# Performance work log

Measured on AMD Instinct MI355X. Metric: run time of the kernel, lower is better.

The kernel has to match this reference:

```python
import jax, jax.numpy as jnp
import numpy as np

HEADS = 8
EPS = 1e-5


def _layernorm(x, g, b):
    mu = jnp.mean(x, axis=-1, keepdims=True)
    var = jnp.mean(jnp.square(x - mu), axis=-1, keepdims=True)
    return (x - mu) * jax.lax.rsqrt(var + EPS) * g + b


def setup_inputs() -> dict:
    key = jax.random.key(0)
    ks = jax.random.split(key, 10)
    B, S, D = 4, 2048, 256
    d_ff = 2 * D
    s = 0.02
    return {
        "x": jax.random.normal(ks[0], (B, S, D), dtype=jnp.float32),
        "ln1_g": jnp.ones((D,), jnp.float32),
        "ln1_b": jnp.zeros((D,), jnp.float32),
        "w_qkv": jax.random.normal(ks[1], (3 * D, D), jnp.float32) * s,
        "b_qkv": jnp.zeros((3 * D,), jnp.float32),
        "w_proj": jax.random.normal(ks[2], (D, D), jnp.float32) * s,
        "b_proj": jnp.zeros((D,), jnp.float32),
        "ln2_g": jnp.ones((D,), jnp.float32),
        "ln2_b": jnp.zeros((D,), jnp.float32),
        "w1": jax.random.normal(ks[3], (d_ff, D), jnp.float32) * s,
        "b1": jnp.zeros((d_ff,), jnp.float32),
        "w2": jax.random.normal(ks[4], (D, d_ff), jnp.float32) * s,
        "b2": jnp.zeros((D,), jnp.float32),
    }


def reference(x, ln1_g, ln1_b, w_qkv, b_qkv, w_proj, b_proj,
              ln2_g, ln2_b, w1, b1, w2, b2):
    B, S, D = x.shape
    H = HEADS
    dh = D // H
    scale = dh ** -0.5

    # --- attention sublayer (pre-LN) ---
    y = _layernorm(x, ln1_g, ln1_b)
    qkv = y @ w_qkv.T + b_qkv                       # [B,S,3D]
    qkv = qkv.reshape(B, S, 3, H, dh)
    q = jnp.transpose(qkv[:, :, 0], (0, 2, 1, 3))   # [B,H,S,dh]
    k = jnp.transpose(qkv[:, :, 1], (0, 2, 1, 3))
    v = jnp.transpose(qkv[:, :, 2], (0, 2, 1, 3))
    attn = jax.nn.softmax(jnp.einsum('bhsd,bhtd->bhst', q, k) * scale, axis=-1)
    ctx = jnp.einsum('bhst,bhtd->bhsd', attn, v)    # [B,H,S,dh]
    ctx = jnp.transpose(ctx, (0, 2, 1, 3)).reshape(B, S, D)
    x = x + ctx @ w_proj.T + b_proj

    # --- FFN sublayer (pre-LN) ---
    y = _layernorm(x, ln2_g, ln2_b)
    h = jax.nn.silu(y @ w1.T + b1)                  # [B,S,2D]
    x = x + h @ w2.T + b2
    return x
```

## Files before the change

kernel.cpp:

```cpp
#include <hip/hip_runtime.h>
#include <cstddef>

constexpr int kB   = 4;
constexpr int kS   = 2048;
constexpr int kD   = 256;
constexpr int kH   = 8;
constexpr int kDH  = 32;
constexpr int kDFF = 512;
constexpr int kM   = kB * kS;
constexpr float kEps = 1e-5f;
constexpr float kScaleL2E = 0.17677669529663687f * 1.4426950408889634f;

typedef float f32x4  __attribute__((ext_vector_type(4)));
typedef short bf16x8 __attribute__((ext_vector_type(8)));
typedef unsigned short u16;
typedef unsigned int   u32;

__device__ inline u16 f2bf(float x) {
    union { float f; unsigned u; } c; c.f = x;
    const unsigned r = c.u + 0x7fffu + ((c.u >> 16) & 1u);
    return (u16)(r >> 16);
}

__device__ inline u32 pk_trunc(float lo, float hi) {
    union { float f; u32 u; } a, b; a.f = lo; b.f = hi;
    return __builtin_amdgcn_perm(b.u, a.u, 0x07060302u);
}

__global__ __launch_bounds__(256)
void ln_kernel(const float* __restrict__ x, const float* __restrict__ g,
               const float* __restrict__ b, u16* __restrict__ y)
{
    const int wave = threadIdx.x >> 6;
    const int lane = threadIdx.x & 63;
    const int row  = blockIdx.x * 4 + wave;
    const float4 v = *(const float4*)&x[(size_t)row * kD + lane * 4];
    float s1 = (v.x + v.y) + (v.z + v.w);
    float s2 = (v.x * v.x + v.y * v.y) + (v.z * v.z + v.w * v.w);
    #pragma unroll
    for (int off = 1; off < 64; off <<= 1) {
        s1 += __shfl_xor(s1, off);
        s2 += __shfl_xor(s2, off);
    }
    const float mu  = s1 * (1.0f / kD);
    const float var = s2 * (1.0f / kD) - mu * mu;
    const float inv = rsqrtf(var + kEps);
    const float4 g4 = *(const float4*)&g[lane * 4];
    const float4 b4 = *(const float4*)&b[lane * 4];
    *(ushort4*)&y[(size_t)row * kD + lane * 4] = make_ushort4(
        f2bf((v.x - mu) * inv * g4.x + b4.x),
        f2bf((v.y - mu) * inv * g4.y + b4.y),
        f2bf((v.z - mu) * inv * g4.z + b4.z),
        f2bf((v.w - mu) * inv * g4.w + b4.w));
}

template<int NT, int OUTMODE, bool RES, int KTOT, int MLOOP>
__global__ __launch_bounds__(256)
void gemm_bf16(const u16* __restrict__ A, const float* __restrict__ Wf,
               const float* __restrict__ bias, const float* __restrict__ res,
               float* __restrict__ Cf, u16* __restrict__ Cb,
               u16* __restrict__ KbP, u16* __restrict__ VtP, int N)
{
    constexpr int BSTR = KTOT + 4;
    __shared__ u16 Bs[NT * BSTR];
    const int tid  = threadIdx.x;
    const int wave = tid >> 6;
    const int lane = tid & 63;
    const int quad = lane >> 4;
    const int l16  = lane & 15;
    const int mbase = blockIdx.x * (64 * MLOOP);
    const int n0 = blockIdx.y * NT;

    {
        constexpr int ITS = (NT * KTOT) / 1024;
        #pragma unroll
        for (int it = 0; it < ITS; ++it) {
            const int e   = it * 1024 + tid * 4;
            const int row = e / KTOT;
            const int col = e & (KTOT - 1);
            const float4 wv = *(const float4*)&Wf[(size_t)(n0 + row) * KTOT + col];
            *(ushort4*)&Bs[row * BSTR + col] = make_ushort4(
                f2bf(wv.x), f2bf(wv.y), f2bf(wv.z), f2bf(wv.w));
        }
    }
    __syncthreads();

    #pragma unroll 1
    for (int mi = 0; mi < MLOOP; ++mi) {
        const int m0 = mbase + mi * 64;

        f32x4 acc[NT / 16];
        #pragma unroll
        for (int ni = 0; ni < NT / 16; ++ni) acc[ni] = {0.f, 0.f, 0.f, 0.f};

        const u16* arow = &A[(size_t)(m0 + wave * 16 + l16) * KTOT];
        #pragma unroll 4
        for (int k0 = 0; k0 < KTOT; k0 += 32) {
            const bf16x8 a = *(const bf16x8*)&arow[k0 + quad * 8];
            #pragma unroll
            for (int ni = 0; ni < NT / 16; ++ni) {
                const bf16x8 bf = *(const bf16x8*)&Bs[(ni * 16 + l16) * BSTR + k0 + quad * 8];
                acc[ni] = __builtin_amdgcn_mfma_f32_16x16x32_bf16(a, bf, acc[ni], 0, 0, 0);
            }
        }

        #pragma unroll
        for (int ni = 0; ni < NT / 16; ++ni) {
            const float bias_v = bias[n0 + ni * 16 + l16];
            #pragma unroll
            for (int r = 0; r < 4; ++r) {
                const int m = m0 + wave * 16 + quad * 4 + r;
                float v = acc[ni][r] + bias_v;
                if (OUTMODE == 0) {
                    const int n = n0 + ni * 16 + l16;
                    if (RES) v += res[(size_t)m * N + n];
                    Cf[(size_t)m * N + n] = v;
                } else if (OUTMODE == 1) {
                    const int n = n0 + ni * 16 + l16;
                    v = v / (1.0f + __expf(-v));
                    Cb[(size_t)m * N + n] = f2bf(v);
                } else {
                    const int rgn = n0 >> 8;
                    const int nl  = (n0 & 255) + ni * 16 + l16;
                    const int hh  = nl >> 5, dh = nl & 31;
                    const int bb  = m >> 11, s = m & (kS - 1);
                    const int bh  = bb * kH + hh;
                    if (rgn == 0)
                        Cb[((size_t)bh * kS + s) * kDH + dh] = f2bf(v * kScaleL2E);
                    else if (rgn == 1)
                        KbP[((size_t)bh * kS + s) * kDH + dh] = f2bf(v);
                    else {
                        const int sp = (s & ~63) | (((s & 15) << 2) | ((s >> 4) & 3));
                        VtP[(((size_t)bh * (kS / 8) + (sp >> 3)) * kDH + dh) * 8 + (sp & 7)] = f2bf(v);
                    }
                }
            }
        }
    }
}

constexpr int kPStrU = 72;

__global__ __launch_bounds__(256)
void attn_kernel(const u16* __restrict__ Qb, const u16* __restrict__ Kb,
                 const u16* __restrict__ Vp, u16* __restrict__ ctx)
{
    __shared__ __align__(16) u16 pbuf[4][32 * kPStrU];
    const int tid  = threadIdx.x;
    const int wave = tid >> 6;
    const int lane = tid & 63;
    const int quad = lane >> 4;
    const int l16  = lane & 15;
    const int n    = blockIdx.x;
    const int bh   = (n & 7) * 4 + ((n >> 3) & 3);
    const int b    = bh >> 3;
    const int h    = bh & 7;
    const int qsub = wave >> 1;
    const int half = wave & 1;
    const int q0 = (n >> 5) * 64 + qsub * 32;

    bf16x8 aq[2];
    aq[0] = *(const bf16x8*)&Qb[((size_t)bh * kS + q0 + l16) * kDH + quad * 8];
    aq[1] = *(const bf16x8*)&Qb[((size_t)bh * kS + q0 + 16 + l16) * kDH + quad * 8];

    const u16* Kbase = Kb + (size_t)bh * kS * kDH;
    const u16* Vbase = Vp + (size_t)bh * kS * kDH;
    u16* pw = pbuf[wave];

    f32x4 O[2][2] = {};
    f32x4 lp[2] = {};
    const f32x4 zz = {0.f, 0.f, 0.f, 0.f};

    const int kbeg = half * (kS / 2);
    #pragma unroll 1
    for (int kt = kbeg; kt < kbeg + kS / 2; kt += 64) {
        bf16x8 kf[4];
        #pragma unroll
        for (int kg = 0; kg < 4; ++kg)
            kf[kg] = *(const bf16x8*)
                &Kbase[(size_t)(kt + kg * 16 + l16) * kDH + quad * 8];
        bf16x8 vf[2][2];
        #pragma unroll
        for (int ks = 0; ks < 2; ++ks)
            #pragma unroll
            for (int nf = 0; nf < 2; ++nf)
                vf[ks][nf] = *(const bf16x8*)
                    &Vbase[(size_t)((((kt + ks * 32 + quad * 8) >> 3) * kDH
                                     + nf * 16 + l16) << 3)];

        #pragma unroll
        for (int qb = 0; qb < 2; ++qb) {
            f32x4 S[4];
            #pragma unroll
            for (int kg = 0; kg < 4; ++kg)
                S[kg] = __builtin_amdgcn_mfma_f32_16x16x32_bf16(aq[qb], kf[kg], zz, 0, 0, 0);
            #pragma unroll
            for (int r = 0; r < 4; ++r) {
                const float e0 = exp2f(S[0][r]);
                const float e1 = exp2f(S[1][r]);
                const float e2 = exp2f(S[2][r]);
                const float e3 = exp2f(S[3][r]);
                lp[qb][r] += (e0 + e1) + (e2 + e3);
                uint2 pk;
                pk.x = pk_trunc(e0, e1);
                pk.y = pk_trunc(e2, e3);
                *(uint2*)&pw[(qb * 16 + quad * 4 + r) * kPStrU + l16 * 4] = pk;
            }
        }

        #pragma unroll
        for (int qb = 0; qb < 2; ++qb)
            #pragma unroll
            for (int ks = 0; ks < 2; ++ks) {
                const bf16x8 pA = *(const bf16x8*)
                    &pw[(qb * 16 + l16) * kPStrU + ks * 32 + quad * 8];
                O[qb][0] = __builtin_amdgcn_mfma_f32_16x16x32_bf16(pA, vf[ks][0], O[qb][0], 0, 0, 0);
                O[qb][1] = __builtin_amdgcn_mfma_f32_16x16x32_bf16(pA, vf[ks][1], O[qb][1], 0, 0, 0);
            }
    }

    #pragma unroll
    for (int off = 1; off < 16; off <<= 1)
        #pragma unroll
        for (int qb = 0; qb < 2; ++qb)
            #pragma unroll
            for (int r = 0; r < 4; ++r)
                lp[qb][r] += __shfl_xor(lp[qb][r], off);

    __syncthreads();
    float* cb = (float*)&pbuf[0][0] + qsub * (32 * 33);
    if (half == 1) {
        #pragma unroll
        for (int qb = 0; qb < 2; ++qb)
            #pragma unroll
            for (int r = 0; r < 4; ++r) {
                const int row = qb * 16 + quad * 4 + r;
                cb[row * 33 + l16]      = O[qb][0][r];
                cb[row * 33 + 16 + l16] = O[qb][1][r];
                if (l16 == 0) cb[row * 33 + 32] = lp[qb][r];
            }
    }
    __syncthreads();
    if (half == 0) {
        #pragma unroll
        for (int qb = 0; qb < 2; ++qb)
            #pragma unroll
            for (int r = 0; r < 4; ++r) {
                const int row = qb * 16 + quad * 4 + r;
                const float l   = lp[qb][r] + cb[row * 33 + 32];
                const float inv = 1.0f / l;
                const float o0 = O[qb][0][r] + cb[row * 33 + l16];
                const float o1 = O[qb][1][r] + cb[row * 33 + 16 + l16];
                const int q = q0 + row;
                u16* crow = ctx + ((size_t)(b * kS + q)) * kD + h * kDH;
                crow[l16]      = f2bf(o0 * inv);
                crow[16 + l16] = f2bf(o1 * inv);
            }
    }
}

extern "C" void kernel_launch(void* const* d_in, const int* in_sizes, int n_in,
                              void* d_out, int out_size, void* d_ws, size_t ws_size,
                              hipStream_t stream)
{
    const float* x      = (const float*)d_in[0];
    const float* ln1_g  = (const float*)d_in[1];
    const float* ln1_b  = (const float*)d_in[2];
    const float* w_qkv  = (const float*)d_in[3];
    const float* b_qkv  = (const float*)d_in[4];
    const float* w_proj = (const float*)d_in[5];
    const float* b_proj = (const float*)d_in[6];
    const float* ln2_g  = (const float*)d_in[7];
    const float* ln2_b  = (const float*)d_in[8];
    const float* w1     = (const float*)d_in[9];
    const float* b1     = (const float*)d_in[10];
    const float* w2     = (const float*)d_in[11];
    const float* b2     = (const float*)d_in[12];
    float* out = (float*)d_out;

    char* ws = (char*)d_ws;
    u16* Qb  = (u16*)ws;
    u16* Kb  = (u16*)(ws + ((size_t)4  << 20));
    u16* Vp  = (u16*)(ws + ((size_t)8  << 20));
    u16* ctx = (u16*)(ws + ((size_t)12 << 20));
    u16* y   = (u16*)(ws + ((size_t)16 << 20));
    u16* h   = (u16*)ws;

    const dim3 blk(256);

    ln_kernel<<<dim3(kM / 4), blk, 0, stream>>>(x, ln1_g, ln1_b, y);
    gemm_bf16<64, 2, false, 256, 4><<<dim3(kM / 256, 12), blk, 0, stream>>>(
        y, w_qkv, b_qkv, nullptr, nullptr, Qb, Kb, Vp, 0);
    attn_kernel<<<dim3(1024), blk, 0, stream>>>(Qb, Kb, Vp, ctx);
    gemm_bf16<32, 0, true, 256, 4><<<dim3(kM / 256, kD / 32), blk, 0, stream>>>(
        ctx, w_proj, b_proj, x, out, nullptr, nullptr, nullptr, kD);
    ln_kernel<<<dim3(kM / 4), blk, 0, stream>>>(out, ln2_g, ln2_b, y);
    gemm_bf16<64, 1, false, 256, 4><<<dim3(kM / 256, kDFF / 64), blk, 0, stream>>>(
        y, w1, b1, nullptr, nullptr, h, nullptr, nullptr, kDFF);
    gemm_bf16<32, 0, true, 512, 4><<<dim3(kM / 256, kD / 32), blk, 0, stream>>>(
        h, w2, b2, out, out, nullptr, nullptr, nullptr, kD);
}
```

Baseline: 195.9 us.

## Compute transposed scores in attention to keep P in registers, drop LDS round-trip

```diff
diff --git a/kernel.cpp b/kernel.cpp
--- a/kernel.cpp
+++ b/kernel.cpp
@@ -130,45 +130,44 @@
                     else if (rgn == 1)
                         KbP[((size_t)bh * kS + s) * kDH + dh] = f2bf(v);
                     else {
-                        const int sp = (s & ~63) | (((s & 15) << 2) | ((s >> 4) & 3));
-                        VtP[(((size_t)bh * (kS / 8) + (sp >> 3)) * kDH + dh) * 8 + (sp & 7)] = f2bf(v);
+                        const int so = s & 31;
+                        const int vq = (so >> 2) & 3;
+                        const int vj = (so & 3) | (((so >> 4) & 1) << 2);
+                        VtP[(((size_t)bh * (kS / 32) + (s >> 5)) * 4 + vq) * 256
+                            + dh * 8 + vj] = f2bf(v);
                     }
                 }
             }
         }
     }
 }
-
-constexpr int kPStrU = 72;
 
 __global__ __launch_bounds__(256)
 void attn_kernel(const u16* __restrict__ Qb, const u16* __restrict__ Kb,
                  const u16* __restrict__ Vp, u16* __restrict__ ctx)
 {
-    __shared__ __align__(16) u16 pbuf[4][32 * kPStrU];
+    __shared__ float cbuf[2][32 * 33];
     const int tid  = threadIdx.x;
     const int wave = tid >> 6;
     const int lane = tid & 63;
     const int quad = lane >> 4;
     const int l16  = lane & 15;
-    const int n    = blockIdx.x;
-    const int bh   = (n & 7) * 4 + ((n >> 3) & 3);
-    const int b    = bh >> 3;
-    const int h    = bh & 7;
+    const int h = blockIdx.y;
+    const int b = blockIdx.z;
+    const int bh = b * kH + h;
     const int qsub = wave >> 1;
     const int half = wave & 1;
-    const int q0 = (n >> 5) * 64 + qsub * 32;
+    const int q0 = blockIdx.x * 64 + qsub * 32;
 
     bf16x8 aq[2];
     aq[0] = *(const bf16x8*)&Qb[((size_t)bh * kS + q0 + l16) * kDH + quad * 8];
     aq[1] = *(const bf16x8*)&Qb[((size_t)bh * kS + q0 + 16 + l16) * kDH + quad * 8];
 
     const u16* Kbase = Kb + (size_t)bh * kS * kDH;
-    const u16* Vbase = Vp + (size_t)bh * kS * kDH;
-    u16* pw = pbuf[wave];
+    const u16* Vbase = Vp + (size_t)bh * (kS * 32);
 
     f32x4 O[2][2] = {};
-    f32x4 lp[2] = {};
+    float lp[2] = {0.f, 0.f};
     const f32x4 zz = {0.f, 0.f, 0.f, 0.f};
 
     const int kbeg = half * (kS / 2);
@@ -185,50 +184,52 @@
             #pragma unroll
             for (int nf = 0; nf < 2; ++nf)
                 vf[ks][nf] = *(const bf16x8*)
-                    &Vbase[(size_t)((((kt + ks * 32 + quad * 8) >> 3) * kDH
-                                     + nf * 16 + l16) << 3)];
+                    &Vbase[(size_t)(((kt >> 5) + ks) * 4 + quad) * 1024
+                           + quad * 0 + (nf * 16 + l16) * 8];
 
         #pragma unroll
         for (int qb = 0; qb < 2; ++qb) {
             f32x4 S[4];
             #pragma unroll
             for (int kg = 0; kg < 4; ++kg)
-                S[kg] = __builtin_amdgcn_mfma_f32_16x16x32_bf16(aq[qb], kf[kg], zz, 0, 0, 0);
+                S[kg] = __builtin_amdgcn_mfma_f32_16x16x32_bf16(kf[kg], aq[qb], zz, 0, 0, 0);
+
+            float e0[8], e1[8];
             #pragma unroll
             for (int r = 0; r < 4; ++r) {
-                const float e0 = exp2f(S[0][r]);
-                const float e1 = exp2f(S[1][r]);
-                const float e2 = exp2f(S[2][r]);
-                const float e3 = exp2f(S[3][r]);
-                lp[qb][r] += (e0 + e1) + (e2 + e3);
-                uint2 pk;
-                pk.x = pk_trunc(e0, e1);
-                pk.y = pk_trunc(e2, e3);
-                *(uint2*)&pw[(qb * 16 + quad * 4 + r) * kPStrU + l16 * 4] = pk;
-            }
+                e0[r]     = exp2f(S[0][r]);
+                e0[4 + r] = exp2f(S[1][r]);
+                e1[r]     = exp2f(S[2][r]);
+                e1[4 + r] = exp2f(S[3][r]);
+            }
+            lp[qb] += ((e0[0] + e0[1]) + (e0[2] + e0[3]))
+                    + ((e0[4] + e0[5]) + (e0[6] + e0[7]))
+                    + ((e1[0] + e1[1]) + (e1[2] + e1[3]))
+                    + ((e1[4] + e1[5]) + (e1[6] + e1[7]));
+            union { u32 u[4]; bf16x8 v; } pA0, pA1;
+            pA0.u[0] = pk_trunc(e0[0], e0[1]);
+            pA0.u[1] = pk_trunc(e0[2], e0[3]);
+            pA0.u[2] = pk_trunc(e0[4], e0[5]);
+            pA0.u[3] = pk_trunc(e0[6], e0[7]);
+            pA1.u[0] = pk_trunc(e1[0], e1[1]);
+            pA1.u[1] = pk_trunc(e1[2], e1[3]);
+            pA1.u[2] = pk_trunc(e1[4], e1[5]);
+            pA1.u[3] = pk_trunc(e1[6], e1[7]);
+
+            O[qb][0] = __builtin_amdgcn_mfma_f32_16x16x32_bf16(pA0.v, vf[0][0], O[qb][0], 0, 0, 0);
+            O[qb][1] = __builtin_amdgcn_mfma_f32_16x16x32_bf16(pA0.v, vf[0][1], O[qb][1], 0, 0, 0);
+            O[qb][0] = __builtin_amdgcn_mfma_f32_16x16x32_bf16(pA1.v, vf[1][0], O[qb][0], 0, 0, 0);
+            O[qb][1] = __builtin_amdgcn_mfma_f32_16x16x32_bf16(pA1.v, vf[1][1], O[qb][1], 0, 0, 0);
         }
-
-        #pragma unroll
-        for (int qb = 0; qb < 2; ++qb)
-            #pragma unroll
-            for (int ks = 0; ks < 2; ++ks) {
-                const bf16x8 pA = *(const bf16x8*)
-                    &pw[(qb * 16 + l16) * kPStrU + ks * 32 + quad * 8];
-                O[qb][0] = __builtin_amdgcn_mfma_f32_16x16x32_bf16(pA, vf[ks][0], O[qb][0], 0, 0, 0);
-                O[qb][1] = __builtin_amdgcn_mfma_f32_16x16x32_bf16(pA, vf[ks][1], O[qb][1], 0, 0, 0);
-            }
     }
 
     #pragma unroll
-    for (int off = 1; off < 16; off <<= 1)
-        #pragma unroll
-        for (int qb = 0; qb < 2; ++qb)
-            #pragma unroll
-            for (int r = 0; r < 4; ++r)
-                lp[qb][r] += __shfl_xor(lp[qb][r], off);
-
-    __syncthreads();
-    float* cb = (float*)&pbuf[0][0] + qsub * (32 * 33);
+    for (int qb = 0; qb < 2; ++qb) {
+        lp[qb] += __shfl_xor(lp[qb], 16);
+        lp[qb] += __shfl_xor(lp[qb], 32);
+    }
+
+    float* cb = cbuf[qsub];
     if (half == 1) {
         #pragma unroll
         for (int qb = 0; qb < 2; ++qb)
@@ -237,7 +238,8 @@
                 const int row = qb * 16 + quad * 4 + r;
                 cb[row * 33 + l16]      = O[qb][0][r];
                 cb[row * 33 + 16 + l16] = O[qb][1][r];
-                if (l16 == 0) cb[row * 33 + 32] = lp[qb][r];
+                if (l16 == 0)
+                    cb[row * 33 + 32] = __shfl(lp[qb], quad * 4 + r);
             }
     }
     __syncthreads();
@@ -247,8 +249,8 @@
             #pragma unroll
             for (int r = 0; r < 4; ++r) {
                 const int row = qb * 16 + quad * 4 + r;
-                const float l   = lp[qb][r] + cb[row * 33 + 32];
-                const float inv = 1.0f / l;
+                const float lq  = __shfl(lp[qb], quad * 4 + r) + cb[row * 33 + 32];
+                const float inv = 1.0f / lq;
                 const float o0 = O[qb][0][r] + cb[row * 33 + l16];
                 const float o1 = O[qb][1][r] + cb[row * 33 + 16 + l16];
                 const int q = q0 + row;
@@ -289,14 +291,14 @@
     const dim3 blk(256);
 
     ln_kernel<<<dim3(kM / 4), blk, 0, stream>>>(x, ln1_g, ln1_b, y);
-    gemm_bf16<64, 2, false, 256, 4><<<dim3(kM / 256, 12), blk, 0, stream>>>(
+    gemm_bf16<64, 2, false, 256, 2><<<dim3(kM / 128, 12), blk, 0, stream>>>(
         y, w_qkv, b_qkv, nullptr, nullptr, Qb, Kb, Vp, 0);
-    attn_kernel<<<dim3(1024), blk, 0, stream>>>(Qb, Kb, Vp, ctx);
-    gemm_bf16<32, 0, true, 256, 4><<<dim3(kM / 256, kD / 32), blk, 0, stream>>>(
+    attn_kernel<<<dim3(kS / 64, kH, kB), blk, 0, stream>>>(Qb, Kb, Vp, ctx);
+    gemm_bf16<32, 0, true, 256, 2><<<dim3(kM / 128, kD / 32), blk, 0, stream>>>(
         ctx, w_proj, b_proj, x, out, nullptr, nullptr, nullptr, kD);
     ln_kernel<<<dim3(kM / 4), blk, 0, stream>>>(out, ln2_g, ln2_b, y);
-    gemm_bf16<64, 1, false, 256, 4><<<dim3(kM / 256, kDFF / 64), blk, 0, stream>>>(
+    gemm_bf16<64, 1, false, 256, 2><<<dim3(kM / 128, kDFF / 64), blk, 0, stream>>>(
         y, w1, b1, nullptr, nullptr, h, nullptr, nullptr, kDFF);
-    gemm_bf16<32, 0, true, 512, 4><<<dim3(kM / 256, kD / 32), blk, 0, stream>>>(
+    gemm_bf16<32, 0, true, 512, 2><<<dim3(kM / 128, kD / 32), blk, 0, stream>>>(
         h, w2, b2, out, out, nullptr, nullptr, nullptr, kD);
 }
```

Result: faster. 178.2 us (-9.1%).
